# Kernel tuning notes

Hardware: AMD Instinct MI355X
Metric: run time of the kernel (lower is better)

## Reference

```python
import jax, jax.numpy as jnp
import numpy as np

EMBED_DIM = 1024
ATTEN_DIM = 64


def setup_inputs() -> dict:
    key = jax.random.key(0)
    k_x, k_q, k_k, k_v = jax.random.split(key, 4)
    B, S = 4, 4096
    scale = 1.0 / np.sqrt(EMBED_DIM)
    x = jax.random.normal(k_x, (B, S, EMBED_DIM), dtype=jnp.float32)
    # torch nn.Linear weights are [out_features, in_features]
    Wq = jax.random.normal(k_q, (ATTEN_DIM, EMBED_DIM), dtype=jnp.float32) * scale
    Wk = jax.random.normal(k_k, (ATTEN_DIM, EMBED_DIM), dtype=jnp.float32) * scale
    Wv = jax.random.normal(k_v, (ATTEN_DIM, EMBED_DIM), dtype=jnp.float32) * scale
    return {"x": x, "Wq": Wq, "Wk": Wk, "Wv": Wv}


def reference(x, Wq, Wk, Wv):
    # q, k, v: [B, S, D]
    q = jnp.einsum('bse,de->bsd', x, Wq)
    k = jnp.einsum('bse,de->bsd', x, Wk)
    v = jnp.einsum('bse,de->bsd', x, Wv)
    d = k.shape[-1]
    scores = jnp.einsum('bsd,btd->bst', q, k) / jnp.sqrt(jnp.float32(d))
    S = x.shape[1]
    causal = jnp.tril(jnp.ones((S, S), dtype=bool))
    scores = jnp.where(causal[None, :, :], scores, -jnp.inf)
    attn = jax.nn.softmax(scores, axis=-1)
    return jnp.einsum('bst,btd->bsd', attn, v)
```

## Files before the change

kernel.cpp:

```cpp
#include <hip/hip_runtime.h>
#include <hip/hip_bf16.h>
#include <stdint.h>

typedef __attribute__((ext_vector_type(8))) short  short8;
typedef __attribute__((ext_vector_type(4))) short  short4v;
typedef __attribute__((ext_vector_type(4))) float  float4v;

#define MFMA16(a, b, c) __builtin_amdgcn_mfma_f32_16x16x32_bf16((a), (b), (c), 0, 0, 0)

#define S_LEN  4096
#define NBATCH 4
#define EMB    1024
#define DD     64
#define NROWS  (NBATCH * S_LEN)
#define SCL2   0.1803368801111204f

#define AS1 const __attribute__((address_space(1))) unsigned int*
#define AS3 __attribute__((address_space(3))) unsigned int*

static __device__ __forceinline__ short f2bf(float f) {
  uint32_t u = __float_as_uint(f);
  return (short)((u + 0x7FFFu + ((u >> 16) & 1u)) >> 16);
}
static __device__ __forceinline__ unsigned pk2(float a, float b) {
  union { __hip_bfloat162 h; unsigned u; } z;
  z.h = __float22bfloat162_rn(make_float2(a, b));
  return z.u;
}
static __device__ __forceinline__ short8 cvt8(float4v a, float4v b) {
  union { unsigned u[4]; short8 s; } z;
  z.u[0] = pk2(a[0], a[1]); z.u[1] = pk2(a[2], a[3]);
  z.u[2] = pk2(b[0], b[1]); z.u[3] = pk2(b[2], b[3]);
  return z.s;
}

__global__ void wcvt_kernel(const float* __restrict__ Wq, const float* __restrict__ Wk,
                            const float* __restrict__ Wv, short* __restrict__ Wb2) {
  const int t   = blockIdx.x * 256 + threadIdx.x;
  const int row = t >> 7;
  const int k   = (t & 127) * 8;
  const float* src = (row < 64) ? (Wq + (size_t)row * EMB)
                   : (row < 128) ? (Wk + (size_t)(row - 64) * EMB)
                                 : (Wv + (size_t)(row - 128) * EMB);
  const float sc = (row < 64) ? SCL2 : 1.0f;
  float4v a = *(const float4v*)(src + k);
  float4v b = *(const float4v*)(src + k + 4);
#pragma unroll
  for (int i = 0; i < 4; ++i) { a[i] *= sc; b[i] *= sc; }
  *(short8*)(Wb2 + (((k >> 5) * 192 + row) << 5) + (k & 31)) = cvt8(a, b);
}

__global__ __launch_bounds__(256, 2) void qkv_kernel(
    const float* __restrict__ x, const short* __restrict__ Wb2,
    short* __restrict__ Qb, short* __restrict__ Kb, short* __restrict__ Vt) {
  __shared__ float As[2][2048];
  __shared__ short Bs[2][12288];

  const int tid  = threadIdx.x;
  const int w    = tid >> 6;
  const int lane = tid & 63;
  const int ln   = lane & 15;
  const int quad = lane >> 4;
  const int m0   = blockIdx.x * 32;
  const int wr   = w & 1;
  const int wc   = w >> 1;

  const int tA0 = 2 * w, tA1 = 2 * w + 1;
  const float* xA0 = x + (size_t)(m0 + ((tA0 >> 2) << 4) + (lane >> 2)) * EMB
                       + ((tA0 & 3) * 4 + (lane & 3)) * 4;
  const float* xA1 = x + (size_t)(m0 + ((tA1 >> 2) << 4) + (lane >> 2)) * EMB
                       + ((tA1 & 3) * 4 + (lane & 3)) * 4;
  const short* wB = Wb2 + (size_t)(6 * w) * 512 + lane * 8;

#define STAGE(S, BUF) do {                                                      \
    __builtin_amdgcn_global_load_lds((AS1)(xA0 + (S) * 64),                     \
        (AS3)&As[BUF][tA0 * 256], 16, 0, 0);                                    \
    __builtin_amdgcn_global_load_lds((AS1)(xA1 + (S) * 64),                     \
        (AS3)&As[BUF][tA1 * 256], 16, 0, 0);                                    \
    _Pragma("unroll")                                                           \
    for (int j = 0; j < 6; ++j)                                                 \
      __builtin_amdgcn_global_load_lds((AS1)(wB + (size_t)(S) * 12288 + j * 512),\
          (AS3)&Bs[BUF][(6 * w + j) * 512], 16, 0, 0);                          \
  } while (0)

  const float4v zz = {0.f, 0.f, 0.f, 0.f};
  float4v acc[6] = {zz, zz, zz, zz, zz, zz};

  STAGE(0, 0);
  int buf = 0;
  for (int s = 0; s < 16; ++s) {
    __syncthreads();
    if (s + 1 < 16) STAGE(s + 1, buf ^ 1);
    short8 aF[2];
#pragma unroll
    for (int h = 0; h < 2; ++h) {
      const int ai = (wr * 4 + 2 * h + (quad >> 1)) * 256 + (ln * 4 + (quad & 1) * 2) * 4;
      const float4v lo = *(const float4v*)&As[buf][ai];
      const float4v hi = *(const float4v*)&As[buf][ai + 4];
      aF[h] = cvt8(lo, hi);
    }
#pragma unroll
    for (int f = 0; f < 6; ++f) {
      const int cf = wc * 6 + f;
      const short8 b0 = *(const short8*)&Bs[buf][(cf * 16 + ln) * 32 + quad * 8];
      const short8 b1 = *(const short8*)&Bs[buf][6144 + (cf * 16 + ln) * 32 + quad * 8];
      if (wc == 0 || f < 2) {
        acc[f] = MFMA16(aF[0], b0, acc[f]);
        acc[f] = MFMA16(aF[1], b1, acc[f]);
      } else {
        acc[f] = MFMA16(b0, aF[0], acc[f]);
        acc[f] = MFMA16(b1, aF[1], acc[f]);
      }
    }
    buf ^= 1;
  }
#undef STAGE

  const int b  = m0 >> 12;
  const int sb = m0 & (S_LEN - 1);
  if (wc == 0) {
#pragma unroll
    for (int f = 0; f < 6; ++f)
#pragma unroll
      for (int r = 0; r < 4; ++r) {
        const int row = m0 + wr * 16 + quad * 4 + r;
        if (f < 4) Qb[(size_t)row * DD + f * 16 + ln] = f2bf(acc[f][r]);
        else       Kb[(size_t)row * DD + (f - 4) * 16 + ln] = f2bf(acc[f][r]);
      }
  } else {
#pragma unroll
    for (int f = 0; f < 2; ++f)
#pragma unroll
      for (int r = 0; r < 4; ++r) {
        const int row = m0 + wr * 16 + quad * 4 + r;
        Kb[(size_t)row * DD + 32 + f * 16 + ln] = f2bf(acc[f][r]);
      }
#pragma unroll
    for (int f = 2; f < 6; ++f)
#pragma unroll
      for (int r = 0; r < 4; ++r) {
        const int d = (f - 2) * 16 + quad * 4 + r;
        Vt[((size_t)b * DD + d) * S_LEN + sb + wr * 16 + ln] = f2bf(acc[f][r]);
      }
  }
}

#define PSTRW 68

__global__ __launch_bounds__(512, 2) void attn_kernel(
    const short* __restrict__ Qb, const short* __restrict__ Kb,
    const short* __restrict__ Vt, float* __restrict__ out) {
  __shared__ float sbuf[8][32 * PSTRW];
  __shared__ float llds[8][32];

  const int tid  = threadIdx.x;
  const int w    = tid >> 6;
  const int lane = tid & 63;
  const int ln   = lane & 15;
  const int quad = lane >> 4;
  const int g    = blockIdx.x;
  const int u    = g & 255;
  const int half = g >> 8;
  const int b    = u & 3;
  const int jj   = u >> 2;
  const int band = half ? (127 - jj) : jj;
  const short* Kbase = Kb + (size_t)b * S_LEN * DD;
  const short* Vbase = Vt + (size_t)b * DD * S_LEN;
  float* pw = &sbuf[w][0];
  const float4v zz = {0.f, 0.f, 0.f, 0.f};

  const int qb  = band * 32;
  const int qg0 = b * S_LEN + qb;

  short8 aQ[2][2];
#pragma unroll
  for (int rfi = 0; rfi < 2; ++rfi)
#pragma unroll
    for (int h = 0; h < 2; ++h)
      aQ[rfi][h] = *(const short8*)(Qb + (size_t)(qg0 + rfi * 16 + ln) * DD + h * 32 + quad * 8);

  float4v o[2][4];
  float lp[2][4];
#pragma unroll
  for (int rfi = 0; rfi < 2; ++rfi)
#pragma unroll
    for (int d = 0; d < 4; ++d) { o[rfi][d] = zz; lp[rfi][d] = 0.f; }

  const int T = (qb + 95) >> 6;

  for (int it = w; it < T; it += 8) {
    const int kv0 = it * 64;
    short8 Kc[4][2];
#pragma unroll
    for (int c = 0; c < 4; ++c)
#pragma unroll
      for (int h = 0; h < 2; ++h)
        Kc[c][h] = *(const short8*)(Kbase + (size_t)(kv0 + c * 16 + ln) * DD + h * 32 + quad * 8);
    short8 Vc[4][2];
#pragma unroll
    for (int d = 0; d < 4; ++d)
#pragma unroll
      for (int h = 0; h < 2; ++h)
        Vc[d][h] = *(const short8*)(Vbase + (size_t)(d * 16 + ln) * S_LEN + kv0 + h * 32 + quad * 8);

    float4v s[2][4];
#pragma unroll
    for (int rfi = 0; rfi < 2; ++rfi)
#pragma unroll
      for (int c = 0; c < 4; ++c) {
        s[rfi][c] = MFMA16(aQ[rfi][0], Kc[c][0], zz);
        s[rfi][c] = MFMA16(aQ[rfi][1], Kc[c][1], s[rfi][c]);
      }

    if ((kv0 + 63) > qb) {
#pragma unroll
      for (int rfi = 0; rfi < 2; ++rfi)
#pragma unroll
        for (int c = 0; c < 4; ++c)
#pragma unroll
          for (int r = 0; r < 4; ++r) {
            float e = __builtin_amdgcn_exp2f(fminf(s[rfi][c][r], 60.0f));
            if (kv0 + c * 16 + ln > qb + rfi * 16 + quad * 4 + r) e = 0.f;
            s[rfi][c][r] = e;
          }
    } else {
#pragma unroll
      for (int rfi = 0; rfi < 2; ++rfi)
#pragma unroll
        for (int c = 0; c < 4; ++c)
#pragma unroll
          for (int r = 0; r < 4; ++r)
            s[rfi][c][r] = __builtin_amdgcn_exp2f(fminf(s[rfi][c][r], 60.0f));
    }

#pragma unroll
    for (int rfi = 0; rfi < 2; ++rfi) {
#pragma unroll
      for (int r = 0; r < 4; ++r)
        lp[rfi][r] += s[rfi][0][r] + s[rfi][1][r] + s[rfi][2][r] + s[rfi][3][r];
#pragma unroll
      for (int c = 0; c < 4; ++c)
#pragma unroll
        for (int r = 0; r < 4; ++r)
          pw[(rfi * 16 + quad * 4 + r) * PSTRW + c * 16 + ln] = s[rfi][c][r];
    }
    asm volatile("s_waitcnt lgkmcnt(0)" ::: "memory");
    short8 aP[2][2];
#pragma unroll
    for (int rfi = 0; rfi < 2; ++rfi)
#pragma unroll
      for (int h = 0; h < 2; ++h) {
        const float4v lo = *(const float4v*)&pw[(rfi * 16 + ln) * PSTRW + h * 32 + quad * 8];
        const float4v hi = *(const float4v*)&pw[(rfi * 16 + ln) * PSTRW + h * 32 + quad * 8 + 4];
        aP[rfi][h] = cvt8(lo, hi);
      }
#pragma unroll
    for (int rfi = 0; rfi < 2; ++rfi)
#pragma unroll
      for (int d = 0; d < 4; ++d) {
        o[rfi][d] = MFMA16(aP[rfi][0], Vc[d][0], o[rfi][d]);
        o[rfi][d] = MFMA16(aP[rfi][1], Vc[d][1], o[rfi][d]);
      }
  }

#pragma unroll
  for (int rfi = 0; rfi < 2; ++rfi)
#pragma unroll
    for (int r = 0; r < 4; ++r) {
      float lr = lp[rfi][r];
      lr += __shfl_xor(lr, 1);
      lr += __shfl_xor(lr, 2);
      lr += __shfl_xor(lr, 4);
      lr += __shfl_xor(lr, 8);
      if (ln == 0) llds[w][rfi * 16 + quad * 4 + r] = lr;
#pragma unroll
      for (int d = 0; d < 4; ++d)
        pw[(rfi * 16 + quad * 4 + r) * 64 + d * 16 + ln] = o[rfi][d][r];
    }
  __syncthreads();

#pragma unroll
  for (int jx = 0; jx < 4; ++jx) {
    const int idx = tid + jx * 512;
    const int row = idx >> 6, col = idx & 63;
    float sum = 0.f, lt = 0.f;
#pragma unroll
    for (int wi = 0; wi < 8; ++wi) {
      sum += sbuf[wi][row * 64 + col];
      lt  += llds[wi][row];
    }
    out[(size_t)(qg0 + row) * DD + col] = sum * __builtin_amdgcn_rcpf(lt);
  }
}

extern "C" void kernel_launch(void* const* d_in, const int* in_sizes, int n_in,
                              void* d_out, int out_size, void* d_ws, size_t ws_size,
                              hipStream_t stream) {
  const float* x  = (const float*)d_in[0];
  const float* Wq = (const float*)d_in[1];
  const float* Wk = (const float*)d_in[2];
  const float* Wv = (const float*)d_in[3];

  short* Qb  = (short*)d_ws;
  short* Kb  = Qb + (size_t)NROWS * DD;
  short* Vt  = Kb + (size_t)NROWS * DD;
  short* Wb2 = Vt + (size_t)NROWS * DD;

  wcvt_kernel<<<dim3(96), dim3(256), 0, stream>>>(Wq, Wk, Wv, Wb2);
  qkv_kernel<<<dim3(NROWS / 32), dim3(256), 0, stream>>>(x, Wb2, Qb, Kb, Vt);
  attn_kernel<<<dim3(NBATCH * 128), dim3(512), 0, stream>>>(Qb, Kb, Vt, (float*)d_out);
}
```

Before: 156.3 us.

## Shrink attention blocks to 16-row query bands with 4 waves each

Each attention block now handles 16 query rows with 4 waves instead of 32 rows with 8 waves, and the grid grows to 1024 blocks. Work balance changes as well: batches alternate ascending and descending band order instead of pairing halves. The aim is more blocks for better CU occupancy and load balance under the causal mask. The cost is that each K/V tile loaded from global memory now feeds half as many query rows, so K/V traffic per unit of work roughly doubles.

```diff
diff --git a/kernel.cpp b/kernel.cpp
--- a/kernel.cpp
+++ b/kernel.cpp
@@ -147,11 +147,11 @@
 
 #define PSTRW 68
 
-__global__ __launch_bounds__(512, 2) void attn_kernel(
+__global__ __launch_bounds__(256, 2) void attn_kernel(
     const short* __restrict__ Qb, const short* __restrict__ Kb,
     const short* __restrict__ Vt, float* __restrict__ out) {
-  __shared__ float sbuf[8][32 * PSTRW];
-  __shared__ float llds[8][32];
+  __shared__ float sbuf[4][16 * PSTRW];
+  __shared__ float llds[4][16];
 
   const int tid  = threadIdx.x;
   const int w    = tid >> 6;
@@ -160,35 +160,29 @@
   const int quad = lane >> 4;
   const int g    = blockIdx.x;
   const int u    = g & 255;
-  const int half = g >> 8;
-  const int b    = u & 3;
-  const int jj   = u >> 2;
-  const int band = half ? (127 - jj) : jj;
+  const int b    = g >> 8;
+  const int band = (b & 1) ? (255 - u) : u;
   const short* Kbase = Kb + (size_t)b * S_LEN * DD;
   const short* Vbase = Vt + (size_t)b * DD * S_LEN;
   float* pw = &sbuf[w][0];
   const float4v zz = {0.f, 0.f, 0.f, 0.f};
 
-  const int qb  = band * 32;
+  const int qb  = band * 16;
   const int qg0 = b * S_LEN + qb;
 
-  short8 aQ[2][2];
-#pragma unroll
-  for (int rfi = 0; rfi < 2; ++rfi)
-#pragma unroll
-    for (int h = 0; h < 2; ++h)
-      aQ[rfi][h] = *(const short8*)(Qb + (size_t)(qg0 + rfi * 16 + ln) * DD + h * 32 + quad * 8);
-
-  float4v o[2][4];
-  float lp[2][4];
-#pragma unroll
-  for (int rfi = 0; rfi < 2; ++rfi)
-#pragma unroll
-    for (int d = 0; d < 4; ++d) { o[rfi][d] = zz; lp[rfi][d] = 0.f; }
-
-  const int T = (qb + 95) >> 6;
-
-  for (int it = w; it < T; it += 8) {
+  short8 aQ[2];
+#pragma unroll
+  for (int h = 0; h < 2; ++h)
+    aQ[h] = *(const short8*)(Qb + (size_t)(qg0 + ln) * DD + h * 32 + quad * 8);
+
+  float4v o[4];
+  float lp[4];
+#pragma unroll
+  for (int d = 0; d < 4; ++d) { o[d] = zz; lp[d] = 0.f; }
+
+  const int T = (qb + 79) >> 6;
+
+  for (int it = w; it < T; it += 4) {
     const int kv0 = it * 64;
     short8 Kc[4][2];
 #pragma unroll
@@ -203,89 +197,75 @@
       for (int h = 0; h < 2; ++h)
         Vc[d][h] = *(const short8*)(Vbase + (size_t)(d * 16 + ln) * S_LEN + kv0 + h * 32 + quad * 8);
 
-    float4v s[2][4];
-#pragma unroll
-    for (int rfi = 0; rfi < 2; ++rfi)
-#pragma unroll
-      for (int c = 0; c < 4; ++c) {
-        s[rfi][c] = MFMA16(aQ[rfi][0], Kc[c][0], zz);
-        s[rfi][c] = MFMA16(aQ[rfi][1], Kc[c][1], s[rfi][c]);
-      }
+    float4v s[4];
+#pragma unroll
+    for (int c = 0; c < 4; ++c) {
+      s[c] = MFMA16(aQ[0], Kc[c][0], zz);
+      s[c] = MFMA16(aQ[1], Kc[c][1], s[c]);
+    }
 
     if ((kv0 + 63) > qb) {
 #pragma unroll
-      for (int rfi = 0; rfi < 2; ++rfi)
-#pragma unroll
-        for (int c = 0; c < 4; ++c)
-#pragma unroll
-          for (int r = 0; r < 4; ++r) {
-            float e = __builtin_amdgcn_exp2f(fminf(s[rfi][c][r], 60.0f));
-            if (kv0 + c * 16 + ln > qb + rfi * 16 + quad * 4 + r) e = 0.f;
-            s[rfi][c][r] = e;
-          }
+      for (int c = 0; c < 4; ++c)
+#pragma unroll
+        for (int r = 0; r < 4; ++r) {
+          float e = __builtin_amdgcn_exp2f(fminf(s[c][r], 60.0f));
+          if (kv0 + c * 16 + ln > qb + quad * 4 + r) e = 0.f;
+          s[c][r] = e;
+        }
     } else {
 #pragma unroll
-      for (int rfi = 0; rfi < 2; ++rfi)
-#pragma unroll
-        for (int c = 0; c < 4; ++c)
-#pragma unroll
-          for (int r = 0; r < 4; ++r)
-            s[rfi][c][r] = __builtin_amdgcn_exp2f(fminf(s[rfi][c][r], 60.0f));
-    }
-
-#pragma unroll
-    for (int rfi = 0; rfi < 2; ++rfi) {
+      for (int c = 0; c < 4; ++c)
+#pragma unroll
+        for (int r = 0; r < 4; ++r)
+          s[c][r] = __builtin_amdgcn_exp2f(fminf(s[c][r], 60.0f));
+    }
+
+#pragma unroll
+    for (int r = 0; r < 4; ++r)
+      lp[r] += s[0][r] + s[1][r] + s[2][r] + s[3][r];
+#pragma unroll
+    for (int c = 0; c < 4; ++c)
 #pragma unroll
       for (int r = 0; r < 4; ++r)
-        lp[rfi][r] += s[rfi][0][r] + s[rfi][1][r] + s[rfi][2][r] + s[rfi][3][r];
-#pragma unroll
-      for (int c = 0; c < 4; ++c)
-#pragma unroll
-        for (int r = 0; r < 4; ++r)
-          pw[(rfi * 16 + quad * 4 + r) * PSTRW + c * 16 + ln] = s[rfi][c][r];
-    }
+        pw[(quad * 4 + r) * PSTRW + c * 16 + ln] = s[c][r];
+
     asm volatile("s_waitcnt lgkmcnt(0)" ::: "memory");
-    short8 aP[2][2];
-#pragma unroll
-    for (int rfi = 0; rfi < 2; ++rfi)
-#pragma unroll
-      for (int h = 0; h < 2; ++h) {
-        const float4v lo = *(const float4v*)&pw[(rfi * 16 + ln) * PSTRW + h * 32 + quad * 8];
-        const float4v hi = *(const float4v*)&pw[(rfi * 16 + ln) * PSTRW + h * 32 + quad * 8 + 4];
-        aP[rfi][h] = cvt8(lo, hi);
-      }
-#pragma unroll
-    for (int rfi = 0; rfi < 2; ++rfi)
-#pragma unroll
-      for (int d = 0; d < 4; ++d) {
-        o[rfi][d] = MFMA16(aP[rfi][0], Vc[d][0], o[rfi][d]);
-        o[rfi][d] = MFMA16(aP[rfi][1], Vc[d][1], o[rfi][d]);
-      }
-  }
-
-#pragma unroll
-  for (int rfi = 0; rfi < 2; ++rfi)
-#pragma unroll
-    for (int r = 0; r < 4; ++r) {
-      float lr = lp[rfi][r];
-      lr += __shfl_xor(lr, 1);
-      lr += __shfl_xor(lr, 2);
-      lr += __shfl_xor(lr, 4);
-      lr += __shfl_xor(lr, 8);
-      if (ln == 0) llds[w][rfi * 16 + quad * 4 + r] = lr;
-#pragma unroll
-      for (int d = 0; d < 4; ++d)
-        pw[(rfi * 16 + quad * 4 + r) * 64 + d * 16 + ln] = o[rfi][d][r];
-    }
+    short8 aP[2];
+#pragma unroll
+    for (int h = 0; h < 2; ++h) {
+      const float4v lo = *(const float4v*)&pw[ln * PSTRW + h * 32 + quad * 8];
+      const float4v hi = *(const float4v*)&pw[ln * PSTRW + h * 32 + quad * 8 + 4];
+      aP[h] = cvt8(lo, hi);
+    }
+#pragma unroll
+    for (int d = 0; d < 4; ++d) {
+      o[d] = MFMA16(aP[0], Vc[d][0], o[d]);
+      o[d] = MFMA16(aP[1], Vc[d][1], o[d]);
+    }
+  }
+
+#pragma unroll
+  for (int r = 0; r < 4; ++r) {
+    float lr = lp[r];
+    lr += __shfl_xor(lr, 1);
+    lr += __shfl_xor(lr, 2);
+    lr += __shfl_xor(lr, 4);
+    lr += __shfl_xor(lr, 8);
+    if (ln == 0) llds[w][quad * 4 + r] = lr;
+#pragma unroll
+    for (int d = 0; d < 4; ++d)
+      pw[(quad * 4 + r) * 64 + d * 16 + ln] = o[d][r];
+  }
   __syncthreads();
 
 #pragma unroll
   for (int jx = 0; jx < 4; ++jx) {
-    const int idx = tid + jx * 512;
+    const int idx = tid + jx * 256;
     const int row = idx >> 6, col = idx & 63;
     float sum = 0.f, lt = 0.f;
 #pragma unroll
-    for (int wi = 0; wi < 8; ++wi) {
+    for (int wi = 0; wi < 4; ++wi) {
       sum += sbuf[wi][row * 64 + col];
       lt  += llds[wi][row];
     }
@@ -308,5 +288,5 @@
 
   wcvt_kernel<<<dim3(96), dim3(256), 0, stream>>>(Wq, Wk, Wv, Wb2);
   qkv_kernel<<<dim3(NROWS / 32), dim3(256), 0, stream>>>(x, Wb2, Qb, Kb, Vt);
-  attn_kernel<<<dim3(NBATCH * 128), dim3(512), 0, stream>>>(Qb, Kb, Vt, (float*)d_out);
-}
+  attn_kernel<<<dim3(NBATCH * 256), dim3(256), 0, stream>>>(Qb, Kb, Vt, (float*)d_out);
+}
```

New measurement: 182.1 us. 16.6% more time.

## Switch attention to 32x32 MFMA with transposed scores and register-only P repacking

Applied to the files above, without the earlier changes.

The attention inner loop moves from 16x16x32 MFMA tiles to 32x32x16 MFMA and computes S^T (K as the A operand, Q as the B operand), so each lane holds the scores for a single query row. The probability tile is converted to bf16 in registers with v_cvt_pk_bf16_f32 and rearranged with permlane32_swap, which removes the LDS store/load round trip and the lgkmcnt wait on every KV tile. The row-sum becomes a single per-lane accumulator reduced with one cross-half shuffle. In exchange it depends on gfx950-specific instructions and on the 32x32 accumulator layout, and it raises per-lane register pressure.

```diff
diff --git a/kernel.cpp b/kernel.cpp
--- a/kernel.cpp
+++ b/kernel.cpp
@@ -5,8 +5,11 @@
 typedef __attribute__((ext_vector_type(8))) short  short8;
 typedef __attribute__((ext_vector_type(4))) short  short4v;
 typedef __attribute__((ext_vector_type(4))) float  float4v;
+typedef __attribute__((ext_vector_type(16))) float f32x16;
+typedef __attribute__((ext_vector_type(2))) unsigned int uint2v;
 
 #define MFMA16(a, b, c) __builtin_amdgcn_mfma_f32_16x16x32_bf16((a), (b), (c), 0, 0, 0)
+#define MFMA32(a, b, c) __builtin_amdgcn_mfma_f32_32x32x16_bf16((a), (b), (c), 0, 0, 0)
 
 #define S_LEN  4096
 #define NBATCH 4
@@ -145,19 +148,17 @@
   }
 }
 
-#define PSTRW 68
-
 __global__ __launch_bounds__(512, 2) void attn_kernel(
     const short* __restrict__ Qb, const short* __restrict__ Kb,
     const short* __restrict__ Vt, float* __restrict__ out) {
-  __shared__ float sbuf[8][32 * PSTRW];
+  __shared__ float sbuf[8][2048];
   __shared__ float llds[8][32];
 
   const int tid  = threadIdx.x;
   const int w    = tid >> 6;
   const int lane = tid & 63;
-  const int ln   = lane & 15;
-  const int quad = lane >> 4;
+  const int l31  = lane & 31;
+  const int hi   = lane >> 5;
   const int g    = blockIdx.x;
   const int u    = g & 255;
   const int half = g >> 8;
@@ -166,117 +167,105 @@
   const int band = half ? (127 - jj) : jj;
   const short* Kbase = Kb + (size_t)b * S_LEN * DD;
   const short* Vbase = Vt + (size_t)b * DD * S_LEN;
-  float* pw = &sbuf[w][0];
-  const float4v zz = {0.f, 0.f, 0.f, 0.f};
-
-  const int qb  = band * 32;
-  const int qg0 = b * S_LEN + qb;
-
-  short8 aQ[2][2];
-#pragma unroll
-  for (int rfi = 0; rfi < 2; ++rfi)
-#pragma unroll
-    for (int h = 0; h < 2; ++h)
-      aQ[rfi][h] = *(const short8*)(Qb + (size_t)(qg0 + rfi * 16 + ln) * DD + h * 32 + quad * 8);
-
-  float4v o[2][4];
-  float lp[2][4];
-#pragma unroll
-  for (int rfi = 0; rfi < 2; ++rfi)
-#pragma unroll
-    for (int d = 0; d < 4; ++d) { o[rfi][d] = zz; lp[rfi][d] = 0.f; }
+
+  const int qb    = band * 32;
+  const int qg0   = b * S_LEN + qb;
+  const int qglob = qb + l31;
+
+  short8 q8[4];
+#pragma unroll
+  for (int dk = 0; dk < 4; ++dk)
+    q8[dk] = *(const short8*)(Qb + (size_t)(qg0 + l31) * DD + dk * 16 + hi * 8);
+
+  f32x16 o0, o1;
+  f32x16 zz16;
+#pragma unroll
+  for (int e = 0; e < 16; ++e) { o0[e] = 0.f; o1[e] = 0.f; zz16[e] = 0.f; }
+  float lp = 0.f;
 
   const int T = (qb + 95) >> 6;
 
   for (int it = w; it < T; it += 8) {
     const int kv0 = it * 64;
-    short8 Kc[4][2];
-#pragma unroll
-    for (int c = 0; c < 4; ++c)
-#pragma unroll
-      for (int h = 0; h < 2; ++h)
-        Kc[c][h] = *(const short8*)(Kbase + (size_t)(kv0 + c * 16 + ln) * DD + h * 32 + quad * 8);
-    short8 Vc[4][2];
-#pragma unroll
-    for (int d = 0; d < 4; ++d)
-#pragma unroll
-      for (int h = 0; h < 2; ++h)
-        Vc[d][h] = *(const short8*)(Vbase + (size_t)(d * 16 + ln) * S_LEN + kv0 + h * 32 + quad * 8);
-
-    float4v s[2][4];
-#pragma unroll
-    for (int rfi = 0; rfi < 2; ++rfi)
-#pragma unroll
-      for (int c = 0; c < 4; ++c) {
-        s[rfi][c] = MFMA16(aQ[rfi][0], Kc[c][0], zz);
-        s[rfi][c] = MFMA16(aQ[rfi][1], Kc[c][1], s[rfi][c]);
-      }
-
-    if ((kv0 + 63) > qb) {
-#pragma unroll
-      for (int rfi = 0; rfi < 2; ++rfi)
-#pragma unroll
-        for (int c = 0; c < 4; ++c)
-#pragma unroll
-          for (int r = 0; r < 4; ++r) {
-            float e = __builtin_amdgcn_exp2f(fminf(s[rfi][c][r], 60.0f));
-            if (kv0 + c * 16 + ln > qb + rfi * 16 + quad * 4 + r) e = 0.f;
-            s[rfi][c][r] = e;
-          }
+    short8 kf[2][4];
+#pragma unroll
+    for (int c = 0; c < 2; ++c)
+#pragma unroll
+      for (int dk = 0; dk < 4; ++dk)
+        kf[c][dk] = *(const short8*)(Kbase + (size_t)(kv0 + c * 32 + l31) * DD + dk * 16 + hi * 8);
+    short8 vf[2][4];
+#pragma unroll
+    for (int df = 0; df < 2; ++df)
+#pragma unroll
+      for (int kc = 0; kc < 4; ++kc)
+        vf[df][kc] = *(const short8*)(Vbase + (size_t)(df * 32 + l31) * S_LEN + kv0 + kc * 16 + hi * 8);
+
+    f32x16 s0 = MFMA32(kf[0][0], q8[0], zz16);
+    f32x16 s1 = MFMA32(kf[1][0], q8[0], zz16);
+#pragma unroll
+    for (int dk = 1; dk < 4; ++dk) {
+      s0 = MFMA32(kf[0][dk], q8[dk], s0);
+      s1 = MFMA32(kf[1][dk], q8[dk], s1);
+    }
+
+    if (kv0 + 63 > qb) {
+#pragma unroll
+      for (int e = 0; e < 16; ++e) {
+        const int kvl = (e & 3) + 8 * (e >> 2) + 4 * hi;
+        float e0 = __builtin_amdgcn_exp2f(fminf(s0[e], 60.0f));
+        if (kv0 + kvl > qglob) e0 = 0.f;
+        float e1 = __builtin_amdgcn_exp2f(fminf(s1[e], 60.0f));
+        if (kv0 + 32 + kvl > qglob) e1 = 0.f;
+        s0[e] = e0; s1[e] = e1;
+        lp += e0 + e1;
+      }
     } else {
 #pragma unroll
-      for (int rfi = 0; rfi < 2; ++rfi)
-#pragma unroll
-        for (int c = 0; c < 4; ++c)
-#pragma unroll
-          for (int r = 0; r < 4; ++r)
-            s[rfi][c][r] = __builtin_amdgcn_exp2f(fminf(s[rfi][c][r], 60.0f));
-    }
-
-#pragma unroll
-    for (int rfi = 0; rfi < 2; ++rfi) {
-#pragma unroll
-      for (int r = 0; r < 4; ++r)
-        lp[rfi][r] += s[rfi][0][r] + s[rfi][1][r] + s[rfi][2][r] + s[rfi][3][r];
-#pragma unroll
-      for (int c = 0; c < 4; ++c)
-#pragma unroll
-        for (int r = 0; r < 4; ++r)
-          pw[(rfi * 16 + quad * 4 + r) * PSTRW + c * 16 + ln] = s[rfi][c][r];
-    }
-    asm volatile("s_waitcnt lgkmcnt(0)" ::: "memory");
-    short8 aP[2][2];
-#pragma unroll
-    for (int rfi = 0; rfi < 2; ++rfi)
-#pragma unroll
-      for (int h = 0; h < 2; ++h) {
-        const float4v lo = *(const float4v*)&pw[(rfi * 16 + ln) * PSTRW + h * 32 + quad * 8];
-        const float4v hi = *(const float4v*)&pw[(rfi * 16 + ln) * PSTRW + h * 32 + quad * 8 + 4];
-        aP[rfi][h] = cvt8(lo, hi);
-      }
-#pragma unroll
-    for (int rfi = 0; rfi < 2; ++rfi)
-#pragma unroll
-      for (int d = 0; d < 4; ++d) {
-        o[rfi][d] = MFMA16(aP[rfi][0], Vc[d][0], o[rfi][d]);
-        o[rfi][d] = MFMA16(aP[rfi][1], Vc[d][1], o[rfi][d]);
-      }
-  }
-
-#pragma unroll
-  for (int rfi = 0; rfi < 2; ++rfi)
-#pragma unroll
-    for (int r = 0; r < 4; ++r) {
-      float lr = lp[rfi][r];
-      lr += __shfl_xor(lr, 1);
-      lr += __shfl_xor(lr, 2);
-      lr += __shfl_xor(lr, 4);
-      lr += __shfl_xor(lr, 8);
-      if (ln == 0) llds[w][rfi * 16 + quad * 4 + r] = lr;
-#pragma unroll
-      for (int d = 0; d < 4; ++d)
-        pw[(rfi * 16 + quad * 4 + r) * 64 + d * 16 + ln] = o[rfi][d][r];
-    }
+      for (int e = 0; e < 16; ++e) {
+        float e0 = __builtin_amdgcn_exp2f(fminf(s0[e], 60.0f));
+        float e1 = __builtin_amdgcn_exp2f(fminf(s1[e], 60.0f));
+        s0[e] = e0; s1[e] = e1;
+        lp += e0 + e1;
+      }
+    }
+
+#define PACK_PV(S, V00, V01, V10, V11) do {                                     \
+    unsigned ua, ub, uc, ud, ue, uf2, ug, uh;                                   \
+    asm("v_cvt_pk_bf16_f32 %0, %1, %2" : "=v"(ua) : "v"((S)[0]),  "v"((S)[1])); \
+    asm("v_cvt_pk_bf16_f32 %0, %1, %2" : "=v"(ub) : "v"((S)[2]),  "v"((S)[3])); \
+    asm("v_cvt_pk_bf16_f32 %0, %1, %2" : "=v"(uc) : "v"((S)[4]),  "v"((S)[5])); \
+    asm("v_cvt_pk_bf16_f32 %0, %1, %2" : "=v"(ud) : "v"((S)[6]),  "v"((S)[7])); \
+    asm("v_cvt_pk_bf16_f32 %0, %1, %2" : "=v"(ue) : "v"((S)[8]),  "v"((S)[9])); \
+    asm("v_cvt_pk_bf16_f32 %0, %1, %2" : "=v"(uf2): "v"((S)[10]), "v"((S)[11]));\
+    asm("v_cvt_pk_bf16_f32 %0, %1, %2" : "=v"(ug) : "v"((S)[12]), "v"((S)[13]));\
+    asm("v_cvt_pk_bf16_f32 %0, %1, %2" : "=v"(uh) : "v"((S)[14]), "v"((S)[15]));\
+    uint2v r0 = __builtin_amdgcn_permlane32_swap(ua, uc, false, false);         \
+    uint2v r1 = __builtin_amdgcn_permlane32_swap(ub, ud, false, false);         \
+    uint2v r2 = __builtin_amdgcn_permlane32_swap(ue, ug, false, false);         \
+    uint2v r3 = __builtin_amdgcn_permlane32_swap(uf2, uh, false, false);        \
+    union { unsigned uu[4]; short8 s8; } p0, p1;                                \
+    p0.uu[0] = r0[0]; p0.uu[1] = r1[0]; p0.uu[2] = r0[1]; p0.uu[3] = r1[1];     \
+    p1.uu[0] = r2[0]; p1.uu[1] = r3[0]; p1.uu[2] = r2[1]; p1.uu[3] = r3[1];     \
+    o0 = MFMA32(p0.s8, (V00), o0);                                              \
+    o0 = MFMA32(p1.s8, (V01), o0);                                              \
+    o1 = MFMA32(p0.s8, (V10), o1);                                              \
+    o1 = MFMA32(p1.s8, (V11), o1);                                              \
+  } while (0)
+
+    PACK_PV(s0, vf[0][0], vf[0][1], vf[1][0], vf[1][1]);
+    PACK_PV(s1, vf[0][2], vf[0][3], vf[1][2], vf[1][3]);
+#undef PACK_PV
+  }
+
+  lp += __shfl_xor(lp, 32);
+  float* pw = &sbuf[w][0];
+#pragma unroll
+  for (int e = 0; e < 16; ++e) {
+    const int ql = (e & 3) + 8 * (e >> 2) + 4 * hi;
+    pw[ql * 64 + l31]      = o0[e];
+    pw[ql * 64 + 32 + l31] = o1[e];
+  }
+  if (hi == 0) llds[w][l31] = lp;
   __syncthreads();
 
 #pragma unroll
```

Result: no change. 155.4 us (-0.6%).
